# Kernel tuning notes

Hardware: AMD Instinct MI355X
Metric: run time of the kernel (lower is better)

Reference implementation:

```python
import jax, jax.numpy as jnp
import numpy as np

B, T, C, H = 2, 2048, 1024, 16
D = C // H            # head dim = 64
MAXREL = 32           # max_relative_position


def setup_inputs() -> dict:
    key = jax.random.key(0)
    ks = jax.random.split(key, 4)
    s = lambda n: 1.0 / np.sqrt(n).astype(np.float32)
    return {
        "x": jax.random.normal(ks[0], (B, T, C), jnp.float32),
        # causal mask, as produced by torch.tril buffer `bias`
        "mask": jnp.tril(jnp.ones((1, 1, T, T), jnp.float32)),
        "w_attn": jax.random.normal(ks[1], (C, 3 * C), jnp.float32) * s(C),
        "b_attn": jnp.zeros((3 * C,), jnp.float32),
        "w_proj": jax.random.normal(ks[2], (C, C), jnp.float32) * s(C),
        "b_proj": jnp.zeros((C,), jnp.float32),
        "rel_k_table": jax.random.normal(ks[3], (2 * MAXREL + 1, D), jnp.float32) * s(D),
    }


def reference(x, mask, w_attn, b_attn, w_proj, b_proj, rel_k_table):
    # qkv projection and head split
    qkv = x @ w_attn + b_attn                              # [B,T,3C]
    q, k, v = jnp.split(qkv, 3, axis=-1)
    to_heads = lambda t: t.reshape(B, T, H, D).transpose(0, 2, 1, 3)  # [B,H,T,D]
    q, k, v = to_heads(q), to_heads(k), to_heads(v)

    # content-content scores
    attn1 = jnp.einsum('bhqd,bhkd->bhqk', q, k)            # [B,H,T,T]

    # content-position scores via relative-position embedding gather
    dist = jnp.arange(T)[None, :] - jnp.arange(T)[:, None]
    idx = jnp.clip(dist, -MAXREL, MAXREL) + MAXREL         # [T,T] in [0, 2*MAXREL]
    rel_k = rel_k_table[idx]                               # [T,T,D]
    attn2 = jnp.einsum('bhqd,qkd->bhqk', q, rel_k)         # [B,H,T,T]

    att = (attn1 + attn2) * (1.0 / np.sqrt(D).astype(np.float32))
    att = jnp.where(mask[:, :, :T, :T] == 0, -jnp.inf, att)
    att = jax.nn.softmax(att, axis=-1)
    att = jnp.nan_to_num(att, nan=0.0)                     # fully-masked rows -> 0
    post_soft_att = att                                    # dropout is identity (eval)

    y = jnp.einsum('bhqk,bhkd->bhqd', att, v)              # [B,H,T,D]
    y = y.transpose(0, 2, 1, 3).reshape(B, T, C)
    y = y @ w_proj + b_proj
    return y, post_soft_att
```

## Files before the change

### kernel.cpp

```cpp
#include <hip/hip_runtime.h>


__global__ __launch_bounds__(256)
void sgemm_bias_kernel(const float* __restrict__ A, const float* __restrict__ B,
                       const float* __restrict__ bias, float* __restrict__ C,
                       int M, int N, int K) {
  __shared__ float As[16 * 128];
  __shared__ float Bs[16 * 128];
  const int tid = threadIdx.x;
  const int tx = tid & 15, ty = tid >> 4;
  const int bm = blockIdx.y * 128, bn = blockIdx.x * 128;

  float acc[8][8] = {{0.f}};

  for (int k0 = 0; k0 < K; k0 += 16) {
#pragma unroll
    for (int j = 0; j < 2; ++j) {
      int f4 = tid + j * 256;
      int m = f4 >> 2, kq = (f4 & 3) << 2;
      float4 va = *(const float4*)&A[(size_t)(bm + m) * K + k0 + kq];
      As[(kq + 0) * 128 + m] = va.x;
      As[(kq + 1) * 128 + m] = va.y;
      As[(kq + 2) * 128 + m] = va.z;
      As[(kq + 3) * 128 + m] = va.w;
      int kr = f4 >> 5, c4 = (f4 & 31) << 2;
      *(float4*)&Bs[kr * 128 + c4] =
          *(const float4*)&B[(size_t)(k0 + kr) * N + bn + c4];
    }
    __syncthreads();
#pragma unroll
    for (int k = 0; k < 16; ++k) {
      float4 a0 = *(const float4*)&As[k * 128 + ty * 4];
      float4 a1 = *(const float4*)&As[k * 128 + 64 + ty * 4];
      float4 b0 = *(const float4*)&Bs[k * 128 + tx * 4];
      float4 b1 = *(const float4*)&Bs[k * 128 + 64 + tx * 4];
      float av[8] = {a0.x, a0.y, a0.z, a0.w, a1.x, a1.y, a1.z, a1.w};
      float bv[8] = {b0.x, b0.y, b0.z, b0.w, b1.x, b1.y, b1.z, b1.w};
#pragma unroll
      for (int i = 0; i < 8; ++i)
#pragma unroll
        for (int j = 0; j < 8; ++j)
          acc[i][j] = fmaf(av[i], bv[j], acc[i][j]);
    }
    __syncthreads();
  }

#pragma unroll
  for (int i = 0; i < 8; ++i) {
    int mrow = bm + ((i < 4) ? (ty * 4 + i) : (64 + ty * 4 + i - 4));
#pragma unroll
    for (int jq = 0; jq < 2; ++jq) {
      int c = bn + jq * 64 + tx * 4;
      float4 o;
      o.x = acc[i][jq * 4 + 0] + bias[c + 0];
      o.y = acc[i][jq * 4 + 1] + bias[c + 1];
      o.z = acc[i][jq * 4 + 2] + bias[c + 2];
      o.w = acc[i][jq * 4 + 3] + bias[c + 3];
      *(float4*)&C[(size_t)mrow * N + c] = o;
    }
  }
}

__global__ __launch_bounds__(256)
void relproj_kernel(const float* __restrict__ qkv, const float* __restrict__ tbl_g,
                    float* __restrict__ proj) {
  __shared__ float tbl[65 * 65];
  __shared__ float qsh[4 * 64];
  const int tid = threadIdx.x;
  for (int i = tid; i < 65 * 64; i += 256) {
    int r = i >> 6, d = i & 63;
    tbl[r * 65 + d] = tbl_g[i];
  }
  const int w = tid >> 6, lane = tid & 63;
  const int rid = blockIdx.x * 4 + w;
  const int b = rid >> 15, h = (rid >> 11) & 15, q = rid & 2047;
  qsh[w * 64 + lane] =
      qkv[(size_t)(b * 2048 + q) * 3072 + h * 64 + lane];
  __syncthreads();
  float acc = 0.f;
#pragma unroll
  for (int d = 0; d < 64; ++d)
    acc = fmaf(qsh[w * 64 + d], tbl[lane * 65 + d], acc);
  proj[(size_t)rid * 65 + lane] = acc;
  float part = qsh[w * 64 + lane] * tbl[64 * 65 + lane];
#pragma unroll
  for (int off = 32; off; off >>= 1) part += __shfl_xor(part, off, 64);
  if (lane == 0) proj[(size_t)rid * 65 + 64] = part;
}

__global__ __launch_bounds__(512)
void attn_kernel(const float* __restrict__ qkv, const float* __restrict__ proj,
                 float* __restrict__ att, float* __restrict__ ymid) {
  __shared__ float p_s[16 * 2048];
  __shared__ float kv_s[64 * 68];
  __shared__ float qt[16 * 64];
  __shared__ float pj[16 * 65];
  const int tid = threadIdx.x;
  const int w = tid >> 6, lane = tid & 63;
  const int bh = blockIdx.y;
  const int b = bh >> 4, h = bh & 15;
  const int q0 = blockIdx.x << 4;
  const size_t row_base = (size_t)(b * 2048) * 3072 + h * 64;

  if (tid < 256) {
    int r = tid >> 4, c4 = (tid & 15) << 2;
    *(float4*)&qt[r * 64 + c4] =
        *(const float4*)&qkv[row_base + (size_t)(q0 + r) * 3072 + c4];
  }
  {
    const float* psrc = &proj[((size_t)bh * 2048 + q0) * 65];
    for (int i = tid; i < 16 * 65; i += 512) pj[i] = psrc[i];
  }
  __syncthreads();

  const int r0 = w * 2, r1 = r0 + 1;
  const int qg0 = q0 + r0, qg1 = q0 + r1;
  const int nkt = q0 / 64 + 1;

  float4 q0v[16], q1v[16];
#pragma unroll
  for (int c = 0; c < 16; ++c) {
    q0v[c] = *(float4*)&qt[r0 * 64 + 4 * c];
    q1v[c] = *(float4*)&qt[r1 * 64 + 4 * c];
  }

  float dacc0 = 0.f, dacc1 = 0.f;
  const float* kbase = qkv + row_base + 1024;
  for (int t = 0; t < nkt; ++t) {
    __syncthreads();
#pragma unroll
    for (int j = 0; j < 2; ++j) {
      int f4 = tid + j * 512;
      int kk = f4 >> 4, d4 = (f4 & 15) << 2;
      *(float4*)&kv_s[kk * 68 + d4] =
          *(const float4*)&kbase[(size_t)(t * 64 + kk) * 3072 + d4];
    }
    __syncthreads();
    float a0a = 0.f, a0b = 0.f, a1a = 0.f, a1b = 0.f;
#pragma unroll
    for (int c = 0; c < 16; ++c) {
      float4 kv = *(float4*)&kv_s[lane * 68 + 4 * c];
      a0a = fmaf(q0v[c].x, kv.x, a0a);
      a0b = fmaf(q0v[c].y, kv.y, a0b);
      a0a = fmaf(q0v[c].z, kv.z, a0a);
      a0b = fmaf(q0v[c].w, kv.w, a0b);
      a1a = fmaf(q1v[c].x, kv.x, a1a);
      a1b = fmaf(q1v[c].y, kv.y, a1b);
      a1a = fmaf(q1v[c].z, kv.z, a1a);
      a1b = fmaf(q1v[c].w, kv.w, a1b);
    }
    float acc0 = a0a + a0b, acc1 = a1a + a1b;
    int kg = t * 64 + lane;
    float p0 = 0.f, p1 = 0.f;
    if (kg <= qg0) {
      int dist = qg0 - kg;
      int idx = 32 - (dist > 32 ? 32 : dist);
      p0 = __expf((acc0 + pj[r0 * 65 + idx]) * 0.125f);
      dacc0 += p0;
    }
    if (kg <= qg1) {
      int dist = qg1 - kg;
      int idx = 32 - (dist > 32 ? 32 : dist);
      p1 = __expf((acc1 + pj[r1 * 65 + idx]) * 0.125f);
      dacc1 += p1;
    }
    p_s[r0 * 2048 + kg] = p0;
    p_s[r1 * 2048 + kg] = p1;
  }

#pragma unroll
  for (int off = 32; off; off >>= 1) {
    dacc0 += __shfl_xor(dacc0, off, 64);
    dacc1 += __shfl_xor(dacc1, off, 64);
  }
  const float inv0 = 1.f / dacc0, inv1 = 1.f / dacc1;

  float* att0 = &att[((size_t)bh * 2048 + qg0) * 2048];
  float* att1 = &att[((size_t)bh * 2048 + qg1) * 2048];

  for (int t = nkt; t < 32; ++t) {
    att0[t * 64 + lane] = 0.f;
    att1[t * 64 + lane] = 0.f;
  }

  const float* vbase = qkv + row_base + 2048;
  float y0a = 0.f, y0b = 0.f, y1a = 0.f, y1b = 0.f;
  for (int t = 0; t < nkt; ++t) {
    __syncthreads();
#pragma unroll
    for (int j = 0; j < 2; ++j) {
      int idx = tid + j * 512;
      int d = idx & 63, k4 = idx >> 6;
      const float* src = &vbase[(size_t)(t * 64 + 4 * k4) * 3072 + d];
      float4 vv;
      vv.x = src[0];
      vv.y = src[3072];
      vv.z = src[6144];
      vv.w = src[9216];
      *(float4*)&kv_s[d * 64 + 4 * (k4 ^ (d & 15))] = vv;
    }
    __syncthreads();
#pragma unroll
    for (int c = 0; c < 16; ++c) {
      float4 vv = *(float4*)&kv_s[lane * 64 + 4 * (c ^ (lane & 15))];
      float4 pb0 = *(float4*)&p_s[r0 * 2048 + t * 64 + 4 * c];
      float4 pb1 = *(float4*)&p_s[r1 * 2048 + t * 64 + 4 * c];
      y0a = fmaf(pb0.x, vv.x, y0a);
      y0b = fmaf(pb0.y, vv.y, y0b);
      y0a = fmaf(pb0.z, vv.z, y0a);
      y0b = fmaf(pb0.w, vv.w, y0b);
      y1a = fmaf(pb1.x, vv.x, y1a);
      y1b = fmaf(pb1.y, vv.y, y1b);
      y1a = fmaf(pb1.z, vv.z, y1a);
      y1b = fmaf(pb1.w, vv.w, y1b);
    }
    att0[t * 64 + lane] = p_s[r0 * 2048 + t * 64 + lane] * inv0;
    att1[t * 64 + lane] = p_s[r1 * 2048 + t * 64 + lane] * inv1;
  }
  ymid[(size_t)(b * 2048 + qg0) * 1024 + h * 64 + lane] = (y0a + y0b) * inv0;
  ymid[(size_t)(b * 2048 + qg1) * 1024 + h * 64 + lane] = (y1a + y1b) * inv1;
}

extern "C" void kernel_launch(void* const* d_in, const int* in_sizes, int n_in,
                              void* d_out, int out_size, void* d_ws, size_t ws_size,
                              hipStream_t stream) {
  const float* x       = (const float*)d_in[0];
  const float* w_attn  = (const float*)d_in[2];
  const float* b_attn  = (const float*)d_in[3];
  const float* w_proj  = (const float*)d_in[4];
  const float* b_proj  = (const float*)d_in[5];
  const float* rel_tbl = (const float*)d_in[6];

  float* out = (float*)d_out;
  float* att = out + (size_t)2 * 2048 * 1024;

  float* qkv  = (float*)d_ws;
  float* proj = qkv + (size_t)2 * 2048 * 3072;
  float* ymid = proj + (size_t)2 * 16 * 2048 * 65;

  sgemm_bias_kernel<<<dim3(24, 32), 256, 0, stream>>>(x, w_attn, b_attn, qkv,
                                                      4096, 3072, 1024);
  relproj_kernel<<<16384, 256, 0, stream>>>(qkv, rel_tbl, proj);
  attn_kernel<<<dim3(128, 32), 512, 0, stream>>>(qkv, proj, att, ymid);
  sgemm_bias_kernel<<<dim3(8, 32), 256, 0, stream>>>(ymid, w_proj, b_proj, out,
                                                     4096, 1024, 1024);
}
```

Baseline: 1.778 ms.

## Replace FP32 SIMT GEMMs with split-bf16 MFMA GEMMs for projections

Both linear projections now run on matrix cores using a three-term bf16 split (hi*hi + hi*lo + lo*hi) to keep close to fp32 accuracy. New kernels convert activations and weights into hi/lo bf16 pairs, with the weights transposed so K is contiguous. The GEMM tiles 128x128 with swizzled LDS and prefetches the next k-slice into registers. This adds conversion passes and extra workspace traffic and lowers precision slightly compared to true fp32.

```diff
diff --git a/kernel.cpp b/kernel.cpp
--- a/kernel.cpp
+++ b/kernel.cpp
@@ -1,62 +1,156 @@
 #include <hip/hip_runtime.h>
 
 
+typedef __bf16 bf16x8 __attribute__((ext_vector_type(8)));
+typedef float f32x4 __attribute__((ext_vector_type(4)));
+typedef unsigned short u16x8 __attribute__((ext_vector_type(8)));
+
+__device__ __forceinline__ unsigned short f2bf(float f) {
+  unsigned u = __float_as_uint(f);
+  u += 0x7fff + ((u >> 16) & 1);
+  return (unsigned short)(u >> 16);
+}
+__device__ __forceinline__ float bf2f(unsigned short s) {
+  return __uint_as_float(((unsigned)s) << 16);
+}
+
 __global__ __launch_bounds__(256)
-void sgemm_bias_kernel(const float* __restrict__ A, const float* __restrict__ B,
-                       const float* __restrict__ bias, float* __restrict__ C,
-                       int M, int N, int K) {
-  __shared__ float As[16 * 128];
-  __shared__ float Bs[16 * 128];
+void cvt_split(const float* __restrict__ in, unsigned short* __restrict__ hi,
+               unsigned short* __restrict__ lo, int n4) {
+  int i = blockIdx.x * 256 + threadIdx.x;
+  if (i >= n4) return;
+  float4 v = ((const float4*)in)[i];
+  ushort4 h, l;
+  h.x = f2bf(v.x); l.x = f2bf(v.x - bf2f(h.x));
+  h.y = f2bf(v.y); l.y = f2bf(v.y - bf2f(h.y));
+  h.z = f2bf(v.z); l.z = f2bf(v.z - bf2f(h.z));
+  h.w = f2bf(v.w); l.w = f2bf(v.w - bf2f(h.w));
+  ((ushort4*)hi)[i] = h;
+  ((ushort4*)lo)[i] = l;
+}
+
+__global__ __launch_bounds__(256)
+void cvt_split_T(const float* __restrict__ in, unsigned short* __restrict__ hiT,
+                 unsigned short* __restrict__ loT, int K, int N) {
+  __shared__ float tile[64][65];
   const int tid = threadIdx.x;
-  const int tx = tid & 15, ty = tid >> 4;
+  const int bc = blockIdx.x * 64;
+  const int br = blockIdx.y * 64;
+#pragma unroll
+  for (int j = 0; j < 4; ++j) {
+    int f = tid + j * 256;
+    int r = f >> 4, c4 = (f & 15) << 2;
+    *(float4*)&tile[r][c4] = *(const float4*)&in[(size_t)(br + r) * N + bc + c4];
+  }
+  __syncthreads();
+#pragma unroll
+  for (int j = 0; j < 4; ++j) {
+    int f = tid + j * 256;
+    int n = f >> 4, k4 = (f & 15) << 2;
+    ushort4 h, l;
+    float v;
+    v = tile[k4 + 0][n]; h.x = f2bf(v); l.x = f2bf(v - bf2f(h.x));
+    v = tile[k4 + 1][n]; h.y = f2bf(v); l.y = f2bf(v - bf2f(h.y));
+    v = tile[k4 + 2][n]; h.z = f2bf(v); l.z = f2bf(v - bf2f(h.z));
+    v = tile[k4 + 3][n]; h.w = f2bf(v); l.w = f2bf(v - bf2f(h.w));
+    size_t o = (size_t)(bc + n) * K + br + k4;
+    *(ushort4*)&hiT[o] = h;
+    *(ushort4*)&loT[o] = l;
+  }
+}
+
+__device__ __forceinline__ int swz(int row, int k) {
+  return row * 32 + ((((k >> 3) ^ row) & 3) << 3) + (k & 7);
+}
+
+__global__ __launch_bounds__(256)
+void mfma_gemm_bias(const unsigned short* __restrict__ Ah,
+                    const unsigned short* __restrict__ Al,
+                    const unsigned short* __restrict__ Bth,
+                    const unsigned short* __restrict__ Btl,
+                    const float* __restrict__ bias, float* __restrict__ C,
+                    int M, int N, int K) {
+  __shared__ unsigned short As_h[128 * 32], As_l[128 * 32];
+  __shared__ unsigned short Bs_h[128 * 32], Bs_l[128 * 32];
+  const int tid = threadIdx.x;
   const int bm = blockIdx.y * 128, bn = blockIdx.x * 128;
-
-  float acc[8][8] = {{0.f}};
-
-  for (int k0 = 0; k0 < K; k0 += 16) {
-#pragma unroll
-    for (int j = 0; j < 2; ++j) {
-      int f4 = tid + j * 256;
-      int m = f4 >> 2, kq = (f4 & 3) << 2;
-      float4 va = *(const float4*)&A[(size_t)(bm + m) * K + k0 + kq];
-      As[(kq + 0) * 128 + m] = va.x;
-      As[(kq + 1) * 128 + m] = va.y;
-      As[(kq + 2) * 128 + m] = va.z;
-      As[(kq + 3) * 128 + m] = va.w;
-      int kr = f4 >> 5, c4 = (f4 & 31) << 2;
-      *(float4*)&Bs[kr * 128 + c4] =
-          *(const float4*)&B[(size_t)(k0 + kr) * N + bn + c4];
-    }
-    __syncthreads();
-#pragma unroll
-    for (int k = 0; k < 16; ++k) {
-      float4 a0 = *(const float4*)&As[k * 128 + ty * 4];
-      float4 a1 = *(const float4*)&As[k * 128 + 64 + ty * 4];
-      float4 b0 = *(const float4*)&Bs[k * 128 + tx * 4];
-      float4 b1 = *(const float4*)&Bs[k * 128 + 64 + tx * 4];
-      float av[8] = {a0.x, a0.y, a0.z, a0.w, a1.x, a1.y, a1.z, a1.w};
-      float bv[8] = {b0.x, b0.y, b0.z, b0.w, b1.x, b1.y, b1.z, b1.w};
-#pragma unroll
-      for (int i = 0; i < 8; ++i)
-#pragma unroll
-        for (int j = 0; j < 8; ++j)
-          acc[i][j] = fmaf(av[i], bv[j], acc[i][j]);
-    }
-    __syncthreads();
-  }
-
-#pragma unroll
-  for (int i = 0; i < 8; ++i) {
-    int mrow = bm + ((i < 4) ? (ty * 4 + i) : (64 + ty * 4 + i - 4));
-#pragma unroll
-    for (int jq = 0; jq < 2; ++jq) {
-      int c = bn + jq * 64 + tx * 4;
-      float4 o;
-      o.x = acc[i][jq * 4 + 0] + bias[c + 0];
-      o.y = acc[i][jq * 4 + 1] + bias[c + 1];
-      o.z = acc[i][jq * 4 + 2] + bias[c + 2];
-      o.w = acc[i][jq * 4 + 3] + bias[c + 3];
-      *(float4*)&C[(size_t)mrow * N + c] = o;
+  const int l = tid & 63, w = tid >> 6;
+  const int wm = (w >> 1) * 64, wn = (w & 1) * 64;
+  const int fr = l & 15, kg = (l >> 4) << 3;
+
+  const int u0 = tid, u1 = tid + 256;
+  const int m0s = u0 >> 2, k0s = (u0 & 3) << 3;
+  const int m1s = u1 >> 2, k1s = (u1 & 3) << 3;
+
+  f32x4 acc[4][4];
+#pragma unroll
+  for (int i = 0; i < 4; ++i)
+#pragma unroll
+    for (int j = 0; j < 4; ++j) {
+      acc[i][j].x = 0.f; acc[i][j].y = 0.f; acc[i][j].z = 0.f; acc[i][j].w = 0.f;
+    }
+
+  u16x8 rah0, rah1, ral0, ral1, rbh0, rbh1, rbl0, rbl1;
+  {
+    const size_t a0 = (size_t)(bm + m0s) * K + k0s, a1 = (size_t)(bm + m1s) * K + k1s;
+    const size_t b0 = (size_t)(bn + m0s) * K + k0s, b1 = (size_t)(bn + m1s) * K + k1s;
+    rah0 = *(const u16x8*)&Ah[a0];  rah1 = *(const u16x8*)&Ah[a1];
+    ral0 = *(const u16x8*)&Al[a0];  ral1 = *(const u16x8*)&Al[a1];
+    rbh0 = *(const u16x8*)&Bth[b0]; rbh1 = *(const u16x8*)&Bth[b1];
+    rbl0 = *(const u16x8*)&Btl[b0]; rbl1 = *(const u16x8*)&Btl[b1];
+  }
+
+  const int nk = K >> 5;
+  for (int ks = 0; ks < nk; ++ks) {
+    __syncthreads();
+    *(u16x8*)&As_h[swz(m0s, k0s)] = rah0;  *(u16x8*)&As_h[swz(m1s, k1s)] = rah1;
+    *(u16x8*)&As_l[swz(m0s, k0s)] = ral0;  *(u16x8*)&As_l[swz(m1s, k1s)] = ral1;
+    *(u16x8*)&Bs_h[swz(m0s, k0s)] = rbh0;  *(u16x8*)&Bs_h[swz(m1s, k1s)] = rbh1;
+    *(u16x8*)&Bs_l[swz(m0s, k0s)] = rbl0;  *(u16x8*)&Bs_l[swz(m1s, k1s)] = rbl1;
+    __syncthreads();
+    if (ks + 1 < nk) {
+      const int k0 = (ks + 1) << 5;
+      const size_t a0 = (size_t)(bm + m0s) * K + k0 + k0s,
+                   a1 = (size_t)(bm + m1s) * K + k0 + k1s;
+      const size_t b0 = (size_t)(bn + m0s) * K + k0 + k0s,
+                   b1 = (size_t)(bn + m1s) * K + k0 + k1s;
+      rah0 = *(const u16x8*)&Ah[a0];  rah1 = *(const u16x8*)&Ah[a1];
+      ral0 = *(const u16x8*)&Al[a0];  ral1 = *(const u16x8*)&Al[a1];
+      rbh0 = *(const u16x8*)&Bth[b0]; rbh1 = *(const u16x8*)&Bth[b1];
+      rbl0 = *(const u16x8*)&Btl[b0]; rbl1 = *(const u16x8*)&Btl[b1];
+    }
+    bf16x8 ah[4], al[4], bh[4], bl[4];
+#pragma unroll
+    for (int i = 0; i < 4; ++i) {
+      ah[i] = *(bf16x8*)&As_h[swz(wm + i * 16 + fr, kg)];
+      al[i] = *(bf16x8*)&As_l[swz(wm + i * 16 + fr, kg)];
+      bh[i] = *(bf16x8*)&Bs_h[swz(wn + i * 16 + fr, kg)];
+      bl[i] = *(bf16x8*)&Bs_l[swz(wn + i * 16 + fr, kg)];
+    }
+#pragma unroll
+    for (int mi = 0; mi < 4; ++mi)
+#pragma unroll
+      for (int ni = 0; ni < 4; ++ni) {
+        acc[mi][ni] = __builtin_amdgcn_mfma_f32_16x16x32_bf16(
+            ah[mi], bh[ni], acc[mi][ni], 0, 0, 0);
+        acc[mi][ni] = __builtin_amdgcn_mfma_f32_16x16x32_bf16(
+            ah[mi], bl[ni], acc[mi][ni], 0, 0, 0);
+        acc[mi][ni] = __builtin_amdgcn_mfma_f32_16x16x32_bf16(
+            al[mi], bh[ni], acc[mi][ni], 0, 0, 0);
+      }
+  }
+
+#pragma unroll
+  for (int mi = 0; mi < 4; ++mi) {
+    const int rowb = bm + wm + mi * 16 + (l >> 4) * 4;
+#pragma unroll
+    for (int ni = 0; ni < 4; ++ni) {
+      const int col = bn + wn + ni * 16 + fr;
+      const float bv = bias[col];
+      C[(size_t)(rowb + 0) * N + col] = acc[mi][ni].x + bv;
+      C[(size_t)(rowb + 1) * N + col] = acc[mi][ni].y + bv;
+      C[(size_t)(rowb + 2) * N + col] = acc[mi][ni].z + bv;
+      C[(size_t)(rowb + 3) * N + col] = acc[mi][ni].w + bv;
     }
   }
 }
@@ -235,13 +329,24 @@
   float* att = out + (size_t)2 * 2048 * 1024;
 
   float* qkv  = (float*)d_ws;
-  float* proj = qkv + (size_t)2 * 2048 * 3072;
-  float* ymid = proj + (size_t)2 * 16 * 2048 * 65;
-
-  sgemm_bias_kernel<<<dim3(24, 32), 256, 0, stream>>>(x, w_attn, b_attn, qkv,
-                                                      4096, 3072, 1024);
+  float* proj = qkv + (size_t)12582912;
+  float* ymid = proj + (size_t)4259840;
+  unsigned short* xh  = (unsigned short*)(ymid + (size_t)4194304);
+  unsigned short* xl  = xh + (size_t)4194304;
+  unsigned short* wah = xl + (size_t)4194304;
+  unsigned short* wal = wah + (size_t)3145728;
+  unsigned short* wph = wal + (size_t)3145728;
+  unsigned short* wpl = wph + (size_t)1048576;
+
+  cvt_split<<<4096, 256, 0, stream>>>(x, xh, xl, 1048576);
+  cvt_split_T<<<dim3(48, 16), 256, 0, stream>>>(w_attn, wah, wal, 1024, 3072);
+  cvt_split_T<<<dim3(16, 16), 256, 0, stream>>>(w_proj, wph, wpl, 1024, 1024);
+
+  mfma_gemm_bias<<<dim3(24, 32), 256, 0, stream>>>(xh, xl, wah, wal, b_attn,
+                                                   qkv, 4096, 3072, 1024);
   relproj_kernel<<<16384, 256, 0, stream>>>(qkv, rel_tbl, proj);
   attn_kernel<<<dim3(128, 32), 512, 0, stream>>>(qkv, proj, att, ymid);
-  sgemm_bias_kernel<<<dim3(8, 32), 256, 0, stream>>>(ymid, w_proj, b_proj, out,
-                                                     4096, 1024, 1024);
-}
+  cvt_split<<<4096, 256, 0, stream>>>(ymid, xh, xl, 1048576);
+  mfma_gemm_bias<<<dim3(8, 32), 256, 0, stream>>>(xh, xl, wph, wpl, b_proj,
+                                                  out, 4096, 1024, 1024);
+}
```

Result: faster. 1.485 ms (-16.4%).
